# Kernel tuning notes

Hardware: AMD Instinct MI355X
Metric: run time of the kernel (lower is better)

Reference implementation:

```python
import jax, jax.numpy as jnp
import numpy as np

B, L, H, NH, DH, FF, NL, REL = 2, 1024, 256, 8, 32, 1024, 2, 100
SCALE = np.sqrt(DH).astype(np.float32)
EPS = 1e-5


def _ln(x, g, b):
    m = jnp.mean(x, axis=-1, keepdims=True)
    v = jnp.mean(jnp.square(x - m), axis=-1, keepdims=True)
    return (x - m) * jax.lax.rsqrt(v + EPS) * g + b


def setup_inputs() -> dict:
    key = jax.random.key(0)
    ks = jax.random.split(key, 20)
    s = 0.02
    Ek = jax.random.normal(ks[0], (REL, DH), jnp.float32) * s
    Ev = jax.random.normal(ks[1], (REL, DH), jnp.float32) * s
    Ek = Ek.at[0].set(0.0)  # padding_idx=0
    Ev = Ev.at[0].set(0.0)
    return {
        "inputs": jax.random.normal(ks[2], (B, L, H), jnp.float32),
        "Wq": jax.random.normal(ks[3], (NL, H, H), jnp.float32) * s,
        "Wk": jax.random.normal(ks[4], (NL, H, H), jnp.float32) * s,
        "Wv": jax.random.normal(ks[5], (NL, H, H), jnp.float32) * s,
        "Wo": jax.random.normal(ks[6], (NL, H, H), jnp.float32) * s,
        "bo": jnp.zeros((NL, H), jnp.float32),
        "W1": jax.random.normal(ks[7], (NL, H, FF), jnp.float32) * s,
        "b1": jnp.zeros((NL, FF), jnp.float32),
        "W2": jax.random.normal(ks[8], (NL, FF, H), jnp.float32) * s,
        "b2": jnp.zeros((NL, H), jnp.float32),
        "ln1_g": jnp.ones((NL, H), jnp.float32),
        "ln1_b": jnp.zeros((NL, H), jnp.float32),
        "ln2_g": jnp.ones((NL, H), jnp.float32),
        "ln2_b": jnp.zeros((NL, H), jnp.float32),
        "Ek": Ek,
        "Ev": Ev,
        "relations": jax.random.randint(ks[9], (B, L, L), 0, REL, jnp.int32),
        "relations_mask": jax.random.randint(ks[10], (B, L, L), 0, 2, jnp.int32).astype(bool),
    }


def reference(inputs, Wq, Wk, Wv, Wo, bo, W1, b1, W2, b2,
              ln1_g, ln1_b, ln2_g, ln2_b, Ek, Ev, relations, relations_mask):
    # relation embeddings shared across layers and heads: (B,L,L,DH)
    rel_k = Ek[relations]
    rel_v = Ev[relations]
    neg = relations_mask.astype(jnp.float32) * (-1e20)  # (B,L,L)
    x = inputs
    for l in range(NL):
        q = (x @ Wq[l]).reshape(B, L, NH, DH)
        k = (x @ Wk[l]).reshape(B, L, NH, DH)
        v = (x @ Wv[l]).reshape(B, L, NH, DH)
        # scores: q.(k_j + rel_k[i,j]) decomposed to avoid (B,H,L,L,DH)
        e = (jnp.einsum('bihd,bjhd->bhij', q, k)
             + jnp.einsum('bihd,bijd->bhij', q, rel_k)) / SCALE
        e = e + neg[:, None, :, :]
        a = jax.nn.softmax(e, axis=-1)  # (B,NH,L,L)
        o = (jnp.einsum('bhij,bjhd->bihd', a, v)
             + jnp.einsum('bhij,bijd->bihd', a, rel_v)).reshape(B, L, H)
        o = o @ Wo[l] + bo[l]
        x = _ln(x + o, ln1_g[l], ln1_b[l])
        ff = jax.nn.relu(x @ W1[l] + b1[l]) @ W2[l] + b2[l]
        x = _ln(x + ff, ln2_g[l], ln2_b[l])
    return x
```

## Files before the change

### kernel.cpp

```cpp
#include <hip/hip_runtime.h>


typedef unsigned short ushortt;
typedef __attribute__((ext_vector_type(8))) short short8;
typedef __attribute__((ext_vector_type(4))) float f32x4;

__device__ __forceinline__ ushortt f2bf(float f) {
  union { float f; unsigned int u; } c; c.f = f;
  unsigned int r = c.u + 0x7fffu + ((c.u >> 16) & 1u);
  return (ushortt)(r >> 16);
}
__device__ __forceinline__ unsigned int pk2(float a, float b) {
  return (unsigned int)f2bf(a) | ((unsigned int)f2bf(b) << 16);
}

__global__ void wcvt_all_k(const float* __restrict__ Wq, const float* __restrict__ Wk,
                           const float* __restrict__ Wv, const float* __restrict__ Wo,
                           const float* __restrict__ W1, const float* __restrict__ W2,
                           ushortt* __restrict__ wbuf) {
  int i = blockIdx.x * blockDim.x + threadIdx.x;
  int st = gridDim.x * blockDim.x;
  for (; i < 1572864; i += st) {
    int l = (i >= 786432) ? 1 : 0;
    int e = i - (l ? 786432 : 0);
    size_t o_w = (size_t)l * 65536, o_w1 = (size_t)l * 262144;
    float v;
    if (e < 262144) {
      int which = e >> 16;
      int loc = e & 65535;
      int k = loc & 255, n = loc >> 8;
      const float* W = (which == 0) ? Wq : (which == 1) ? Wk : (which == 2) ? Wv : Wo;
      v = W[o_w + ((size_t)k << 8) + n];
    } else if (e < 524288) {
      int loc = e - 262144;
      int k = loc & 255, n = loc >> 8;
      v = W1[o_w1 + ((size_t)k << 10) + n];
    } else {
      int loc = e - 524288;
      int k = loc & 1023, n = loc >> 10;
      v = W2[o_w1 + ((size_t)k << 8) + n];
    }
    wbuf[i] = f2bf(v);
  }
}

__global__ __launch_bounds__(256) void cvt_bf_k(
    const float* __restrict__ in, ushortt* __restrict__ out, int n) {
  int idx = (blockIdx.x * 256 + threadIdx.x) * 8;
  if (idx >= n) return;
  float4 f0 = *(const float4*)(in + idx);
  float4 f1 = *(const float4*)(in + idx + 4);
  uint4 u;
  u.x = pk2(f0.x, f0.y); u.y = pk2(f0.z, f0.w);
  u.z = pk2(f1.x, f1.y); u.w = pk2(f1.z, f1.w);
  *(uint4*)(out + idx) = u;
}

__global__ __launch_bounds__(256) void relpack_k(
    const int* __restrict__ rel, const int* __restrict__ msk,
    unsigned char* __restrict__ relc2,
    const float* __restrict__ Ev, float* __restrict__ EvT,
    const float* __restrict__ Ek, ushortt* __restrict__ ekbf) {
  int g = blockIdx.x * blockDim.x + threadIdx.x;
  const int4* r4 = (const int4*)rel;
  const int4* m4 = (const int4*)msk;
  int4 r = r4[g];
  int4 m = m4[g];
  int b = g >> 18;
  int rem = g & 262143;
  int i = rem >> 8;
  int j4 = (rem & 255) << 2;
  size_t base = ((size_t)b << 20) + ((size_t)(i >> 3) << 13) + (i & 7);
  relc2[base + ((size_t)(j4 + 0) << 3)] = (unsigned char)(m.x ? 128 : r.x);
  relc2[base + ((size_t)(j4 + 1) << 3)] = (unsigned char)(m.y ? 128 : r.y);
  relc2[base + ((size_t)(j4 + 2) << 3)] = (unsigned char)(m.z ? 128 : r.z);
  relc2[base + ((size_t)(j4 + 3) << 3)] = (unsigned char)(m.w ? 128 : r.w);
  if (g < 3200) {
    int d = g / 100, rr = g - d * 100;
    EvT[d * 100 + rr] = Ev[(rr << 5) + d];
  }
  if (g < 3584) {
    int rr = g >> 5, d = g & 31;
    ekbf[g] = (rr < 100) ? f2bf(Ek[(rr << 5) + d]) : (ushortt)0;
  }
}

__device__ __forceinline__ void mgemm_body(
    const ushortt* __restrict__ A, const ushortt* __restrict__ BT,
    const float* __restrict__ bias, size_t boff,
    float* __restrict__ C, ushortt* __restrict__ cbf,
    int m0, int n0, int N, int K, int kbeg, int kend, int relu, int kvmode)
{
  __shared__ ushortt As[64 * 72];
  __shared__ ushortt Bs[64 * 72];
  int tid = threadIdx.x;
  int wv = tid >> 6, lane = tid & 63;
  int quad = lane >> 4, mr = lane & 15;
  int sm = tid >> 2, k16 = (tid & 3) << 4;

  const ushortt* ap = A + (size_t)(m0 + sm) * K + k16;
  const ushortt* bp = BT + (size_t)(n0 + sm) * K + k16;

  uint4 ra0 = *(const uint4*)(ap + kbeg);
  uint4 ra1 = *(const uint4*)(ap + kbeg + 8);
  uint4 rb0 = *(const uint4*)(bp + kbeg);
  uint4 rb1 = *(const uint4*)(bp + kbeg + 8);

  f32x4 acc[4] = {};
  for (int k0 = kbeg; k0 < kend; k0 += 64) {
    *(uint4*)(&As[sm * 72 + k16])     = ra0;
    *(uint4*)(&As[sm * 72 + k16 + 8]) = ra1;
    *(uint4*)(&Bs[sm * 72 + k16])     = rb0;
    *(uint4*)(&Bs[sm * 72 + k16 + 8]) = rb1;
    __syncthreads();
    if (k0 + 64 < kend) {
      ra0 = *(const uint4*)(ap + k0 + 64);
      ra1 = *(const uint4*)(ap + k0 + 72);
      rb0 = *(const uint4*)(bp + k0 + 64);
      rb1 = *(const uint4*)(bp + k0 + 72);
    }
#pragma unroll
    for (int kh = 0; kh < 2; ++kh) {
      short8 af = *(const short8*)(&As[(wv * 16 + mr) * 72 + (kh << 5) + quad * 8]);
#pragma unroll
      for (int nt = 0; nt < 4; ++nt) {
        short8 bf = *(const short8*)(&Bs[(nt * 16 + mr) * 72 + (kh << 5) + quad * 8]);
        acc[nt] = __builtin_amdgcn_mfma_f32_16x16x32_bf16(af, bf, acc[nt], 0, 0, 0);
      }
    }
    __syncthreads();
  }
#pragma unroll
  for (int nt = 0; nt < 4; ++nt) {
#pragma unroll
    for (int r = 0; r < 4; ++r) {
      int m = m0 + wv * 16 + quad * 4 + r;
      int n = n0 + nt * 16 + mr;
      float v = acc[nt][r];
      if (bias) v += bias[boff + n];
      if (relu) v = fmaxf(v, 0.f);
      if (kvmode == 3) {
        int b = m >> 10, i = m & 1023, h = n >> 5, d = n & 31;
        cbf[(size_t)(((b << 3) + h) * 1024 + i) * 32 + d] =
            f2bf(v * 0.17677669529663687f);
      } else if (kvmode == 1) {
        int b = m >> 10, i = m & 1023, h = n >> 5, d = n & 31;
        cbf[(size_t)(((b << 3) + h) * 32 + d) * 1024 + i] = f2bf(v);
      } else if (kvmode == 2) {
        int b = m >> 10, i = m & 1023, h = n >> 5, d = n & 31;
        cbf[(size_t)(((b << 3) + h) * 1024 + i) * 32 + d] = f2bf(v);
      } else if (cbf) {
        cbf[(size_t)m * N + n] = f2bf(v);
      } else {
        C[(size_t)m * N + n] = v;
      }
    }
  }
}

__global__ __launch_bounds__(256) void mgemm_k(
    const ushortt* __restrict__ A, const ushortt* __restrict__ BT,
    const float* __restrict__ bias, size_t boff,
    float* __restrict__ C0, float* __restrict__ C1, ushortt* __restrict__ cbf,
    int N, int K, int relu)
{
  int kidx = blockIdx.z;
  int kc = K / gridDim.z;
  int kbeg = kidx * kc;
  mgemm_body(A, BT, kidx ? nullptr : bias, boff,
             kidx ? C1 : C0, cbf,
             blockIdx.y * 64, blockIdx.x * 64, N, K, kbeg, kbeg + kc, relu, 0);
}

__global__ __launch_bounds__(256) void mqkv_k(
    const ushortt* __restrict__ xbf, const ushortt* __restrict__ WT,
    ushortt* __restrict__ qbf, ushortt* __restrict__ kbf,
    ushortt* __restrict__ vTbf)
{
  int sel = blockIdx.x >> 2;
  const ushortt* BT = WT + (size_t)sel * 65536;
  int mode = (sel == 0) ? 3 : (sel == 1) ? 2 : 1;
  mgemm_body(xbf, BT, nullptr, 0, nullptr,
             (sel == 0) ? qbf : (sel == 1) ? kbf : vTbf,
             blockIdx.y * 64, (blockIdx.x & 3) * 64, 256, 256, 0, 256, 0, mode);
}

__global__ __launch_bounds__(256) void attn_mf8_k(
    const ushortt* __restrict__ qbf, const ushortt* __restrict__ kbf,
    const ushortt* __restrict__ vTbf, const ushortt* __restrict__ ekbf,
    const float* __restrict__ EvT, const unsigned char* __restrict__ relc2,
    ushortt* __restrict__ out)
{
  __shared__ __align__(16) ushortt pbf[8 * 1028];
  __shared__ float expq[800];
  __shared__ float wbin[8 * 108];

  int tid = threadIdx.x;
  int wv = tid >> 6, lane = tid & 63;
  int quad = lane >> 4, mr = lane & 15;
  int bid = blockIdx.x;
  int tile = bid & 127;
  int h = (bid >> 7) & 7;
  int b = bid >> 10;
  int i0 = tile << 3;

  int iqsel = quad & 1;
  int iq = iqsel << 2;
  int jofs = ((quad >> 1) << 4) + mr;
  int jbase = wv << 8;
  const unsigned int* rc2 =
      (const unsigned int*)(relc2 + (((size_t)(b << 7) + tile) << 13));
  unsigned int rcw[8];
#pragma unroll
  for (int t = 0; t < 8; ++t)
    rcw[t] = rc2[(((jbase + (t << 5) + jofs)) << 1) + iqsel];

  for (int p = tid; p < 864; p += 256) wbin[p] = 0.f;

  const ushortt* qsrc = qbf + ((size_t)(b * 8 + h) << 15);
  short8 qf = *(const short8*)(qsrc + (((size_t)i0 + (mr & 7)) << 5) + quad * 8);

  const ushortt* ks = kbf + ((size_t)(b * 8 + h) << 15);
  const ushortt* vs = vTbf + ((size_t)(b * 8 + h) << 15);
  short8 kfa = *(const short8*)(ks + ((size_t)(jbase + mr) << 5) + quad * 8);
  short8 kfb = *(const short8*)(ks + ((size_t)(jbase + 16 + mr) << 5) + quad * 8);

#pragma unroll
  for (int tsel = 0; tsel < 2; ++tsel) {
    int rt = wv + (tsel << 2);
    if (rt <= 6) {
      int r0 = rt << 4;
      short8 ekf = *(const short8*)(ekbf + ((size_t)(r0 + mr) << 5) + quad * 8);
      f32x4 z = {};
      f32x4 eq = __builtin_amdgcn_mfma_f32_16x16x32_bf16(qf, ekf, z, 0, 0, 0);
      if (quad < 2) {
#pragma unroll
        for (int r = 0; r < 4; ++r) {
          int i = quad * 4 + r;
          int rr = r0 + mr;
          if (rr < 100) expq[i * 100 + rr] = __expf(eq[r]);
        }
      }
    }
  }
  __syncthreads();

#pragma unroll
  for (int t = 0; t < 8; ++t) {
    int j0 = jbase + (t << 5);
    short8 ka = kfa, kb = kfb;
    if (t < 7) {
      kfa = *(const short8*)(ks + ((size_t)(j0 + 32 + mr) << 5) + quad * 8);
      kfb = *(const short8*)(ks + ((size_t)(j0 + 48 + mr) << 5) + quad * 8);
    }
    f32x4 z = {};
    f32x4 sa = __builtin_amdgcn_mfma_f32_16x16x32_bf16(qf, ka, z, 0, 0, 0);
    f32x4 sb = __builtin_amdgcn_mfma_f32_16x16x32_bf16(qf, kb, z, 0, 0, 0);
    int j = j0 + jofs;
    unsigned int w = rcw[t];
#pragma unroll
    for (int r = 0; r < 4; ++r) {
      int i = iq + r;
      float sv = (quad >= 2) ? sb[r] : sa[r];
      unsigned int c = (w >> (r << 3)) & 255u;
      float p = 0.f;
      if (c < 128u) {
        p = __expf(sv) * expq[i * 100 + (int)c];
        atomicAdd(&wbin[i * 108 + (int)c], p);
      }
      pbf[i * 1028 + j] = f2bf(p);
    }
  }
  __syncthreads();

  float* pvpart = expq;
  float* pvtot  = expq + 256;
  int d0 = (wv & 1) << 4;
  int k0 = (wv >> 1) << 9;
  int prow = (mr & 7) * 1028;
  f32x4 acc0 = {}, acc1 = {};
  short8 vf = *(const short8*)(vs + ((size_t)(d0 + mr) << 10) + k0 + quad * 8);
#pragma unroll
  for (int kt = 0; kt < 16; ++kt) {
    int kk = k0 + (kt << 5);
    short8 vcur = vf;
    if (kt < 15)
      vf = *(const short8*)(vs + ((size_t)(d0 + mr) << 10) + k0 + ((kt + 1) << 5) + quad * 8);
    short8 pf = *(const short8*)(&pbf[prow + kk + quad * 8]);
    if (kt & 1)
      acc1 = __builtin_amdgcn_mfma_f32_16x16x32_bf16(pf, vcur, acc1, 0, 0, 0);
    else
      acc0 = __builtin_amdgcn_mfma_f32_16x16x32_bf16(pf, vcur, acc0, 0, 0, 0);
  }
  f32x4 acc;
#pragma unroll
  for (int r = 0; r < 4; ++r) acc[r] = acc0[r] + acc1[r];
  if (wv >= 2 && quad < 2) {
#pragma unroll
    for (int r = 0; r < 4; ++r)
      pvpart[((wv & 1) << 7) + (quad * 4 + r) * 16 + mr] = acc[r];
  }
  __syncthreads();
  if (wv < 2 && quad < 2) {
#pragma unroll
    for (int r = 0; r < 4; ++r) {
      int i = quad * 4 + r;
      pvtot[i * 32 + d0 + mr] = acc[r] + pvpart[((wv & 1) << 7) + i * 16 + mr];
    }
  }
  __syncthreads();

  {
    int i = tid >> 5, d = tid & 31;
    const float4* evt = (const float4*)(EvT + d * 100);
    const float4* wb4 = (const float4*)(&wbin[i * 108]);
    float e0 = 0.f, e1 = 0.f, e2 = 0.f, e3 = 0.f;
    float s0 = 0.f, s1 = 0.f, s2 = 0.f, s3 = 0.f;
#pragma unroll
    for (int rq = 0; rq < 25; ++rq) {
      float4 e4 = evt[rq];
      float4 w4 = wb4[rq];
      e0 += w4.x * e4.x; s0 += w4.x;
      e1 += w4.y * e4.y; s1 += w4.y;
      e2 += w4.z * e4.z; s2 += w4.z;
      e3 += w4.w * e4.w; s3 += w4.w;
    }
    float ev = (e0 + e1) + (e2 + e3);
    float den = (s0 + s1) + (s2 + s3);
    out[(((size_t)(b * 1024 + i0 + i) * 8 + h) << 5) + d] =
        f2bf((pvtot[i * 32 + d] + ev) / den);
  }
}

__global__ __launch_bounds__(256) void ln_k(
    const float* __restrict__ x, const float* __restrict__ o,
    const float* __restrict__ o2,
    const float* __restrict__ g, const float* __restrict__ bta, size_t eoff,
    float* __restrict__ xo, ushortt* __restrict__ xbf, float* __restrict__ fout)
{
  int tid = threadIdx.x;
  int lane = tid & 63;
  int row = (blockIdx.x << 2) + (tid >> 6);
  int col = lane << 2;
  size_t base = (size_t)row * 256 + col;

  float4 r = *(const float4*)(x + base);
  float4 ov = *(const float4*)(o + base);
  r.x += ov.x; r.y += ov.y; r.z += ov.z; r.w += ov.w;
  if (o2) {
    float4 o2v = *(const float4*)(o2 + base);
    r.x += o2v.x; r.y += o2v.y; r.z += o2v.z; r.w += o2v.w;
  }
  float s = (r.x + r.y) + (r.z + r.w);
  s += __shfl_xor(s, 1, 64);
  s += __shfl_xor(s, 2, 64);
  s += __shfl_xor(s, 4, 64);
  s += __shfl_xor(s, 8, 64);
  s += __shfl_xor(s, 16, 64);
  s += __shfl_xor(s, 32, 64);
  float mean = s * (1.f / 256.f);
  float dx = r.x - mean, dy = r.y - mean, dz = r.z - mean, dw = r.w - mean;
  float sq = (dx * dx + dy * dy) + (dz * dz + dw * dw);
  sq += __shfl_xor(sq, 1, 64);
  sq += __shfl_xor(sq, 2, 64);
  sq += __shfl_xor(sq, 4, 64);
  sq += __shfl_xor(sq, 8, 64);
  sq += __shfl_xor(sq, 16, 64);
  sq += __shfl_xor(sq, 32, 64);
  float rs = rsqrtf(sq * (1.f / 256.f) + 1e-5f);
  float4 gv = *(const float4*)(g + eoff + col);
  float4 bv = *(const float4*)(bta + eoff + col);
  float4 val;
  val.x = dx * rs * gv.x + bv.x;
  val.y = dy * rs * gv.y + bv.y;
  val.z = dz * rs * gv.z + bv.z;
  val.w = dw * rs * gv.w + bv.w;
  *(float4*)(xo + base) = val;
  uint2 u;
  u.x = pk2(val.x, val.y);
  u.y = pk2(val.z, val.w);
  *(uint2*)(xbf + base) = u;
  if (fout) *(float4*)(fout + base) = val;
}

extern "C" void kernel_launch(void* const* d_in, const int* in_sizes, int n_in,
                              void* d_out, int out_size, void* d_ws, size_t ws_size,
                              hipStream_t stream) {
  const float* inp  = (const float*)d_in[0];
  const float* Wq   = (const float*)d_in[1];
  const float* Wk   = (const float*)d_in[2];
  const float* Wv   = (const float*)d_in[3];
  const float* Wo   = (const float*)d_in[4];
  const float* bo   = (const float*)d_in[5];
  const float* W1   = (const float*)d_in[6];
  const float* b1   = (const float*)d_in[7];
  const float* W2   = (const float*)d_in[8];
  const float* b2   = (const float*)d_in[9];
  const float* ln1g = (const float*)d_in[10];
  const float* ln1b = (const float*)d_in[11];
  const float* ln2g = (const float*)d_in[12];
  const float* ln2b = (const float*)d_in[13];
  const float* Ek   = (const float*)d_in[14];
  const float* Ev   = (const float*)d_in[15];
  const int*   rel  = (const int*)d_in[16];
  const int*   msk  = (const int*)d_in[17];

  const size_t SZ = 524288;
  float* x        = (float*)d_ws;
  float* q        = x + SZ;
  ushortt* kbf    = (ushortt*)(q + SZ);
  ushortt* vTbf   = kbf + SZ;
  ushortt* attnbf = vTbf + SZ;
  ushortt* xbf    = attnbf + SZ;
  float* tmp      = (float*)(xbf + SZ);
  ushortt* wbuf   = (ushortt*)(tmp + SZ);
  unsigned char* relc2 = (unsigned char*)(wbuf + 1572864);
  float* EvT      = (float*)(relc2 + 2097152);
  float* tmp2     = (float*)((char*)EvT + 16384);
  ushortt* inpbf  = (ushortt*)tmp2;
  ushortt* qbf    = (ushortt*)(tmp2 + SZ);
  ushortt* ekbf   = qbf + SZ;
  ushortt* ffh    = (ushortt*)q;

  dim3 blk(256);
  wcvt_all_k<<<3072, blk, 0, stream>>>(Wq, Wk, Wv, Wo, W1, W2, wbuf);
  relpack_k<<<2048, blk, 0, stream>>>(rel, msk, relc2, Ev, EvT, Ek, ekbf);
  cvt_bf_k<<<256, blk, 0, stream>>>(inp, inpbf, 524288);

  for (int l = 0; l < 2; ++l) {
    size_t o_b  = (size_t)l * 256;
    size_t o_b1 = (size_t)l * 1024;
    const ushortt* xinbf = (l == 0) ? inpbf : xbf;
    const float* xin = (l == 0) ? inp : x;
    ushortt* wl = wbuf + (size_t)l * 786432;

    mqkv_k<<<dim3(12, 32), blk, 0, stream>>>(xinbf, wl, qbf, kbf, vTbf);

    attn_mf8_k<<<2048, blk, 0, stream>>>(qbf, kbf, vTbf, ekbf, EvT,
                                         relc2, attnbf);

    mgemm_k<<<dim3(4, 32, 2), blk, 0, stream>>>(attnbf, wl + 196608,
                                                bo, o_b, tmp, tmp2, nullptr,
                                                256, 256, 0);
    ln_k<<<512, blk, 0, stream>>>(xin, tmp, tmp2, ln1g, ln1b, o_b, x, xbf, nullptr);

    mgemm_k<<<dim3(16, 32, 1), blk, 0, stream>>>(xbf, wl + 262144,
                                                 b1, o_b1, nullptr, nullptr, ffh,
                                                 1024, 256, 1);
    mgemm_k<<<dim3(4, 32, 2), blk, 0, stream>>>(ffh, wl + 524288,
                                                b2, o_b, tmp, tmp2, nullptr,
                                                256, 1024, 0);
    ln_k<<<512, blk, 0, stream>>>(x, tmp, tmp2, ln2g, ln2b, o_b, x, xbf,
                                  (l == 1) ? (float*)d_out : nullptr);
  }
}
```

Baseline: 336.1 us.

## Load GEMM tiles straight into LDS with global_load_lds and XOR swizzle

The shared GEMM body now fills its A and B tiles with direct global-to-LDS loads (`global_load_lds`, 16 bytes per lane) instead of staging them through registers. The padded 72-wide shared layout becomes an unpadded 64-wide layout with an XOR column swizzle, which keeps the MFMA fragment reads free of bank conflicts. This cuts VGPR use and the extra LDS store instructions. In exchange it drops the register prefetch of the next k-tile, so global loads no longer overlap with the MFMA work of the current tile.

New measurement: 343.8 us. 2.3% more time.

```diff
diff --git a/kernel.cpp b/kernel.cpp
--- a/kernel.cpp
+++ b/kernel.cpp
@@ -12,6 +12,12 @@
 }
 __device__ __forceinline__ unsigned int pk2(float a, float b) {
   return (unsigned int)f2bf(a) | ((unsigned int)f2bf(b) << 16);
+}
+
+__device__ __forceinline__ void gl16(const ushortt* g, ushortt* l) {
+  __builtin_amdgcn_global_load_lds(
+      (const __attribute__((address_space(1))) unsigned int*)g,
+      (__attribute__((address_space(3))) unsigned int*)l, 16, 0, 0);
 }
 
 __global__ void wcvt_all_k(const float* __restrict__ Wq, const float* __restrict__ Wk,
@@ -91,40 +97,31 @@
     float* __restrict__ C, ushortt* __restrict__ cbf,
     int m0, int n0, int N, int K, int kbeg, int kend, int relu, int kvmode)
 {
-  __shared__ ushortt As[64 * 72];
-  __shared__ ushortt Bs[64 * 72];
+  __shared__ ushortt As[64 * 64];
+  __shared__ ushortt Bs[64 * 64];
   int tid = threadIdx.x;
   int wv = tid >> 6, lane = tid & 63;
   int quad = lane >> 4, mr = lane & 15;
-  int sm = tid >> 2, k16 = (tid & 3) << 4;
-
-  const ushortt* ap = A + (size_t)(m0 + sm) * K + k16;
-  const ushortt* bp = BT + (size_t)(n0 + sm) * K + k16;
-
-  uint4 ra0 = *(const uint4*)(ap + kbeg);
-  uint4 ra1 = *(const uint4*)(ap + kbeg + 8);
-  uint4 rb0 = *(const uint4*)(bp + kbeg);
-  uint4 rb1 = *(const uint4*)(bp + kbeg + 8);
+  int r8 = lane >> 3;
+  int c8 = (lane & 7) ^ r8;
+  int arow = wv << 4;
 
   f32x4 acc[4] = {};
   for (int k0 = kbeg; k0 < kend; k0 += 64) {
-    *(uint4*)(&As[sm * 72 + k16])     = ra0;
-    *(uint4*)(&As[sm * 72 + k16 + 8]) = ra1;
-    *(uint4*)(&Bs[sm * 72 + k16])     = rb0;
-    *(uint4*)(&Bs[sm * 72 + k16 + 8]) = rb1;
+    gl16(A + (size_t)(m0 + arow + r8) * K + k0 + (c8 << 3), &As[arow << 6]);
+    gl16(A + (size_t)(m0 + arow + 8 + r8) * K + k0 + (c8 << 3),
+         &As[(arow + 8) << 6]);
+    gl16(BT + (size_t)(n0 + arow + r8) * K + k0 + (c8 << 3), &Bs[arow << 6]);
+    gl16(BT + (size_t)(n0 + arow + 8 + r8) * K + k0 + (c8 << 3),
+         &Bs[(arow + 8) << 6]);
     __syncthreads();
-    if (k0 + 64 < kend) {
-      ra0 = *(const uint4*)(ap + k0 + 64);
-      ra1 = *(const uint4*)(ap + k0 + 72);
-      rb0 = *(const uint4*)(bp + k0 + 64);
-      rb1 = *(const uint4*)(bp + k0 + 72);
-    }
 #pragma unroll
     for (int kh = 0; kh < 2; ++kh) {
-      short8 af = *(const short8*)(&As[(wv * 16 + mr) * 72 + (kh << 5) + quad * 8]);
+      int colsw = ((kh << 5) + (quad << 3)) ^ ((mr & 7) << 3);
+      short8 af = *(const short8*)(&As[(((wv << 4) + mr) << 6) + colsw]);
 #pragma unroll
       for (int nt = 0; nt < 4; ++nt) {
-        short8 bf = *(const short8*)(&Bs[(nt * 16 + mr) * 72 + (kh << 5) + quad * 8]);
+        short8 bf = *(const short8*)(&Bs[(((nt << 4) + mr) << 6) + colsw]);
         acc[nt] = __builtin_amdgcn_mfma_f32_16x16x32_bf16(af, bf, acc[nt], 0, 0, 0);
       }
     }
```
